# Kernel optimization log

Measured on AMD Instinct MI355X. Metric: run time of the kernel, lower is better.

Reference implementation:

```python
import jax, jax.numpy as jnp
import numpy as np

W_DIM = 512   # latent dim
CH = 512      # number of Fourier channels / output channels
SIZE = 64     # spatial size (square: size[0]=size[1])
SR = 64.0     # sampling_rate
BW = 2.0      # bandwidth
BATCH = 32


def setup_inputs() -> dict:
    key = jax.random.key(0)
    k1, k2, k3, k4, k5 = jax.random.split(key, 5)
    w = jax.random.normal(k1, (BATCH, W_DIM), jnp.float32)
    # affine FC params (weight_init=0 in original; use small random so t varies)
    affine_w = jax.random.normal(k2, (4, W_DIM), jnp.float32) * 0.1
    affine_b = jnp.array([1.0, 0.0, 0.0, 0.0], jnp.float32)
    # channel-mixing weight
    weight = jax.random.normal(k3, (CH, CH), jnp.float32)
    # freqs buffer init: randn, normalized by r*exp(r^2/4), scaled by bandwidth
    f = jax.random.normal(k4, (CH, 2), jnp.float32)
    radii = jnp.sqrt(jnp.sum(f * f, axis=1, keepdims=True))
    f = f / (radii * jnp.exp(radii * radii / 4.0)) * BW
    phases = jax.random.uniform(k5, (CH,), jnp.float32) - 0.5
    return {"w": w, "affine_w": affine_w, "affine_b": affine_b,
            "weight": weight, "freqs": f, "phases": phases}


def reference(w, affine_w, affine_b, weight, freqs, phases):
    # affine FC: FullyConnectedLayer with lr_multiplier=1 -> weight_gain = 1/sqrt(in)
    gain = np.float32(1.0 / np.sqrt(W_DIM))
    t = w @ (affine_w.T * gain) + affine_b                      # [N, 4]
    t = t / jnp.linalg.norm(t[:, :2], axis=1, keepdims=True)
    c, s, tx, ty = t[:, 0], t[:, 1], t[:, 2], t[:, 3]
    # combined transform = m_r @ m_t @ I; top-left 2x2 rotation block:
    R = jnp.stack([jnp.stack([c, -s], -1),
                   jnp.stack([s, c], -1)], axis=1)              # [N, 2, 2]
    # translation column of combined transform (m_r @ m_t)[:, :2, 2]
    trans = jnp.stack([-c * tx + s * ty, -s * tx - c * ty], -1) # [N, 2]
    ph = phases[None, :] + jnp.einsum('cd,nd->nc', freqs, trans)  # [N, C]
    fr = jnp.einsum('cd,nde->nce', freqs, R)                      # [N, C, 2]
    amp = jnp.clip(1.0 - (jnp.linalg.norm(fr, axis=2) - BW) / (SR / 2.0 - BW), 0.0, 1.0)  # [N, C]
    # affine_grid(theta, [1,1,H,W], align_corners=False): base coords (2i+1)/D - 1
    scale = np.float32(0.5 * SIZE / SR)
    xs = ((2.0 * jnp.arange(SIZE, dtype=jnp.float32) + 1.0) / SIZE - 1.0) * scale
    ys = ((2.0 * jnp.arange(SIZE, dtype=jnp.float32) + 1.0) / SIZE - 1.0) * scale
    grid = jnp.stack([jnp.broadcast_to(xs[None, :], (SIZE, SIZE)),
                      jnp.broadcast_to(ys[:, None], (SIZE, SIZE))], axis=-1)  # [H, W, 2]
    # per-pixel Fourier phase: [N, H, W, C]
    x = jnp.einsum('hwd,ncd->nhwc', grid, fr) + ph[:, None, None, :]
    x = jnp.sin(x * np.float32(2.0 * np.pi)) * amp[:, None, None, :]
    # channel projection, then to NCHW
    x = jnp.einsum('nhwc,kc->nkhw', x, weight * np.float32(1.0 / np.sqrt(CH)))
    return x  # [N, CH, H, W]
```

## Files before the change

### kernel.cpp

```cpp
#include <hip/hip_runtime.h>
#include <hip/hip_bf16.h>

#define WDIM 512
#define CHN  512
#define NB   32
#define SZ   64
#define MTOT 4096

typedef __attribute__((ext_vector_type(4))) float f32x4;
typedef __attribute__((ext_vector_type(8))) short short8;
typedef __attribute__((ext_vector_type(4))) int   int4v;
typedef __attribute__((ext_vector_type(4))) float float4v;

__global__ __launch_bounds__(512) void setup_kernel(
    const float* __restrict__ w,
    const float* __restrict__ affine_w,
    const float* __restrict__ affine_b,
    const float* __restrict__ freqs,
    const float* __restrict__ phases,
    float* __restrict__ frx_o, float* __restrict__ fry_o,
    float* __restrict__ pha_o, float* __restrict__ amp_o)
{
    const int n = blockIdx.x;
    const int tid = threadIdx.x;
    __shared__ float red[8][4];
    __shared__ float par[4];

    float wv = w[n * WDIM + tid];
    float p0 = wv * affine_w[0 * WDIM + tid];
    float p1 = wv * affine_w[1 * WDIM + tid];
    float p2 = wv * affine_w[2 * WDIM + tid];
    float p3 = wv * affine_w[3 * WDIM + tid];
    #pragma unroll
    for (int off = 32; off >= 1; off >>= 1) {
        p0 += __shfl_down(p0, off);
        p1 += __shfl_down(p1, off);
        p2 += __shfl_down(p2, off);
        p3 += __shfl_down(p3, off);
    }
    const int wave = tid >> 6;
    if ((tid & 63) == 0) {
        red[wave][0] = p0; red[wave][1] = p1;
        red[wave][2] = p2; red[wave][3] = p3;
    }
    __syncthreads();
    if (tid == 0) {
        const float gain = 0.04419417382415922f;
        float t[4];
        #pragma unroll
        for (int j = 0; j < 4; ++j) {
            float s = 0.0f;
            #pragma unroll
            for (int v = 0; v < 8; ++v) s += red[v][j];
            t[j] = s * gain + affine_b[j];
        }
        float inv = 1.0f / sqrtf(t[0] * t[0] + t[1] * t[1]);
        float c = t[0] * inv, s = t[1] * inv, tx = t[2] * inv, ty = t[3] * inv;
        par[0] = c;
        par[1] = s;
        par[2] = -c * tx + s * ty;
        par[3] = -s * tx - c * ty;
    }
    __syncthreads();
    const float c_ = par[0], s_ = par[1], tr0 = par[2], tr1 = par[3];
    const int ci = tid;
    float fx = freqs[ci * 2 + 0], fy = freqs[ci * 2 + 1];
    float frx = fx * c_ + fy * s_;
    float fry = -fx * s_ + fy * c_;
    float ph = phases[ci] + fx * tr0 + fy * tr1;
    float r = sqrtf(frx * frx + fry * fry);
    float amp = 1.0f - (r - 2.0f) * (1.0f / 30.0f);
    amp = fminf(fmaxf(amp, 0.0f), 1.0f);
    frx_o[n * CHN + ci] = frx;
    fry_o[n * CHN + ci] = fry;
    pha_o[n * CHN + ci] = ph;
    amp_o[n * CHN + ci] = amp;
}

__global__ __launch_bounds__(512) void table_kernel(
    const float* __restrict__ frx, const float* __restrict__ amp,
    float* __restrict__ SA, float* __restrict__ CA)
{
    const int n = blockIdx.x >> 6;
    const int w = blockIdx.x & 63;
    const int c = threadIdx.x;
    float f = frx[n * CHN + c];
    float a = amp[n * CHN + c];
    float xs = (float)(2 * w + 1) * (1.0f / 128.0f) - 0.5f;
    float arg = xs * f;
    size_t idx = ((size_t)(n * 64 + w)) * CHN + c;
    SA[idx] = a * __builtin_amdgcn_sinf(arg);
    CA[idx] = a * __builtin_amdgcn_cosf(arg);
}

__global__ __launch_bounds__(256) void wconv_kernel(
    const float* __restrict__ wsrc, __hip_bfloat16* __restrict__ wbf)
{
    int i = blockIdx.x * 256 + threadIdx.x;
    wbf[i] = __float2bfloat16(wsrc[i] * 0.04419417382415922f);
}

__global__ __launch_bounds__(256, 2) void fused_kernel(
    const float* __restrict__ fry, const float* __restrict__ pha,
    const float* __restrict__ SA, const float* __restrict__ CA,
    const __hip_bfloat16* __restrict__ wbf,
    float* __restrict__ out)
{
    __shared__ __align__(16) __hip_bfloat16 As[128 * 64];
    __shared__ __align__(16) __hip_bfloat16 Bs[128 * 64];
    __shared__ __align__(16) float sB[2][CHN];
    __shared__ __align__(16) float cB[2][CHN];

    const int tid = threadIdx.x;
    const int mb = blockIdx.x * 128;
    const int kb = blockIdx.y * 128;
    const int n  = blockIdx.z;
    const int h0 = mb >> 6;

    #pragma unroll
    for (int u = 0; u < 2; ++u) {
        int c = tid + u * 256;
        float fy = fry[n * CHN + c];
        float ph = pha[n * CHN + c];
        #pragma unroll
        for (int hh = 0; hh < 2; ++hh) {
            float ys = (float)(2 * (h0 + hh) + 1) * (1.0f / 128.0f) - 0.5f;
            float b = ys * fy + ph;
            sB[hh][c] = __builtin_amdgcn_sinf(b);
            cB[hh][c] = __builtin_amdgcn_cosf(b);
        }
    }

    const int lane = tid & 63;
    const int wid  = tid >> 6;
    const int ln15 = lane & 15;
    const int hi4  = lane >> 4;
    const int wk = (wid >> 1) * 64;
    const int wm = (wid & 1) * 64;

    const int cc0 = (tid & 7) * 8;
    const int rb  = tid >> 3;

    const float* saL = SA + ((size_t)(n * 64 + rb)) * CHN + cc0;
    const float* saH = SA + ((size_t)(n * 64 + rb + 32)) * CHN + cc0;
    const float* caL = CA + ((size_t)(n * 64 + rb)) * CHN + cc0;
    const float* caH = CA + ((size_t)(n * 64 + rb + 32)) * CHN + cc0;

    f32x4 acc[4][4];
    #pragma unroll
    for (int a = 0; a < 4; ++a)
        #pragma unroll
        for (int b = 0; b < 4; ++b)
            acc[a][b] = (f32x4)0.0f;

    #pragma unroll 1
    for (int kc = 0; kc < 8; ++kc) {
        const int c0 = kc * 64;
        __syncthreads();

        #pragma unroll
        for (int u = 0; u < 4; ++u) {
            int unit = u * 256 + tid;
            int row = unit >> 3;
            int cbyte = ((unit & 7) << 4) ^ ((row & 7) << 4);
            const __hip_bfloat16* src = wbf + (size_t)(kb + row) * CHN + c0 + (cbyte >> 1);
            char* ldsbase = (char*)Bs + (u * 256 + (wid << 6)) * 16;
            __builtin_amdgcn_global_load_lds(
                (const __attribute__((address_space(1))) unsigned int*)src,
                (__attribute__((address_space(3))) unsigned int*)ldsbase, 16, 0, 0);
        }

        float4v s0 = *(const float4v*)(saL + c0), s1 = *(const float4v*)(saL + c0 + 4);
        float4v s2 = *(const float4v*)(saH + c0), s3 = *(const float4v*)(saH + c0 + 4);
        float4v q0 = *(const float4v*)(caL + c0), q1 = *(const float4v*)(caL + c0 + 4);
        float4v q2 = *(const float4v*)(caH + c0), q3 = *(const float4v*)(caH + c0 + 4);
        #pragma unroll
        for (int i = 0; i < 4; ++i) {
            int m = rb + i * 32;
            int hh = i >> 1;
            float4v As0 = (i & 1) ? s2 : s0, As1 = (i & 1) ? s3 : s1;
            float4v Ac0 = (i & 1) ? q2 : q0, Ac1 = (i & 1) ? q3 : q1;
            float4v Bs0 = *(const float4v*)&sB[hh][c0 + cc0];
            float4v Bs1 = *(const float4v*)&sB[hh][c0 + cc0 + 4];
            float4v Bc0 = *(const float4v*)&cB[hh][c0 + cc0];
            float4v Bc1 = *(const float4v*)&cB[hh][c0 + cc0 + 4];
            union { __hip_bfloat16 h[8]; int4v v; } t;
            #pragma unroll
            for (int j = 0; j < 4; ++j)
                t.h[j] = __float2bfloat16(As0[j] * Bc0[j] + Ac0[j] * Bs0[j]);
            #pragma unroll
            for (int j = 0; j < 4; ++j)
                t.h[4 + j] = __float2bfloat16(As1[j] * Bc1[j] + Ac1[j] * Bs1[j]);
            *(int4v*)((char*)As + m * 128 + ((cc0 * 2) ^ ((m & 7) << 4))) = t.v;
        }
        __syncthreads();

        #pragma unroll
        for (int kk = 0; kk < 2; ++kk) {
            short8 wf[4], ff[4];
            #pragma unroll
            for (int ki = 0; ki < 4; ++ki) {
                int row = wk + ki * 16 + ln15;
                wf[ki] = *(const short8*)((char*)Bs + row * 128 +
                          (((kk * 32 + hi4 * 8) * 2) ^ ((row & 7) << 4)));
            }
            #pragma unroll
            for (int mj = 0; mj < 4; ++mj) {
                int m = wm + mj * 16 + ln15;
                ff[mj] = *(const short8*)((char*)As + m * 128 +
                          (((kk * 32 + hi4 * 8) * 2) ^ ((m & 7) << 4)));
            }
            #pragma unroll
            for (int ki = 0; ki < 4; ++ki)
                #pragma unroll
                for (int mj = 0; mj < 4; ++mj)
                    acc[ki][mj] = __builtin_amdgcn_mfma_f32_16x16x32_bf16(
                        wf[ki], ff[mj], acc[ki][mj], 0, 0, 0);
        }
    }

    #pragma unroll
    for (int ki = 0; ki < 4; ++ki) {
        #pragma unroll
        for (int mj = 0; mj < 4; ++mj) {
            int kg = kb + wk + ki * 16 + hi4 * 4;
            int mg = mb + wm + mj * 16 + ln15;
            float* op = out + ((size_t)n * CHN + kg) * MTOT + mg;
            #pragma unroll
            for (int r = 0; r < 4; ++r)
                op[(size_t)r * MTOT] = acc[ki][mj][r];
        }
    }
}

extern "C" void kernel_launch(void* const* d_in, const int* in_sizes, int n_in,
                              void* d_out, int out_size, void* d_ws, size_t ws_size,
                              hipStream_t stream) {
    const float* w        = (const float*)d_in[0];
    const float* affine_w = (const float*)d_in[1];
    const float* affine_b = (const float*)d_in[2];
    const float* weight   = (const float*)d_in[3];
    const float* freqs    = (const float*)d_in[4];
    const float* phases   = (const float*)d_in[5];
    float* out = (float*)d_out;

    char* ws = (char*)d_ws;
    float* frx = (float*)(ws + 0);
    float* fry = (float*)(ws + 65536);
    float* pha = (float*)(ws + 131072);
    float* amp = (float*)(ws + 196608);
    __hip_bfloat16* wbf = (__hip_bfloat16*)(ws + 262144);
    float* SA = (float*)(ws + 786432);
    float* CA = (float*)(ws + 786432 + 4194304);

    setup_kernel<<<NB, 512, 0, stream>>>(w, affine_w, affine_b, freqs, phases,
                                         frx, fry, pha, amp);
    table_kernel<<<NB * 64, 512, 0, stream>>>(frx, amp, SA, CA);
    wconv_kernel<<<(CHN * CHN) / 256, 256, 0, stream>>>(weight, wbf);

    dim3 grid(MTOT / 128, CHN / 128, NB);
    fused_kernel<<<grid, 256, 0, stream>>>(fry, pha, SA, CA, wbf, out);
}
```

Measured before the change: 120.8 us.

## Double-buffer LDS tiles in fused GEMM and merge table/weight-convert kernels

The fused kernel now keeps two LDS buffers for the feature and weight tiles. It prefetches the next K-chunk (async weight load plus SA/CA global loads) and builds its features while the current chunk's MFMAs run, which drops one barrier per iteration. The table and weight-conversion kernels are merged into one launch to save launch overhead. Doubling the LDS use (about 80KB per block) may limit occupancy under the 2-blocks-per-CU launch bound.

```diff
diff --git a/kernel.cpp b/kernel.cpp
--- a/kernel.cpp
+++ b/kernel.cpp
@@ -77,27 +77,28 @@
     amp_o[n * CHN + ci] = amp;
 }
 
-__global__ __launch_bounds__(512) void table_kernel(
+__global__ __launch_bounds__(512) void prep_kernel(
     const float* __restrict__ frx, const float* __restrict__ amp,
-    float* __restrict__ SA, float* __restrict__ CA)
+    const float* __restrict__ wsrc,
+    float* __restrict__ SA, float* __restrict__ CA,
+    __hip_bfloat16* __restrict__ wbf)
 {
-    const int n = blockIdx.x >> 6;
-    const int w = blockIdx.x & 63;
-    const int c = threadIdx.x;
-    float f = frx[n * CHN + c];
-    float a = amp[n * CHN + c];
-    float xs = (float)(2 * w + 1) * (1.0f / 128.0f) - 0.5f;
-    float arg = xs * f;
-    size_t idx = ((size_t)(n * 64 + w)) * CHN + c;
-    SA[idx] = a * __builtin_amdgcn_sinf(arg);
-    CA[idx] = a * __builtin_amdgcn_cosf(arg);
-}
-
-__global__ __launch_bounds__(256) void wconv_kernel(
-    const float* __restrict__ wsrc, __hip_bfloat16* __restrict__ wbf)
-{
-    int i = blockIdx.x * 256 + threadIdx.x;
-    wbf[i] = __float2bfloat16(wsrc[i] * 0.04419417382415922f);
+    const int b = blockIdx.x;
+    if (b < NB * 64) {
+        const int n = b >> 6;
+        const int w = b & 63;
+        const int c = threadIdx.x;
+        float f = frx[n * CHN + c];
+        float a = amp[n * CHN + c];
+        float xs = (float)(2 * w + 1) * (1.0f / 128.0f) - 0.5f;
+        float arg = xs * f;
+        size_t idx = ((size_t)(n * 64 + w)) * CHN + c;
+        SA[idx] = a * __builtin_amdgcn_sinf(arg);
+        CA[idx] = a * __builtin_amdgcn_cosf(arg);
+    } else {
+        int i = (b - NB * 64) * 512 + threadIdx.x;
+        wbf[i] = __float2bfloat16(wsrc[i] * 0.04419417382415922f);
+    }
 }
 
 __global__ __launch_bounds__(256, 2) void fused_kernel(
@@ -106,8 +107,8 @@
     const __hip_bfloat16* __restrict__ wbf,
     float* __restrict__ out)
 {
-    __shared__ __align__(16) __hip_bfloat16 As[128 * 64];
-    __shared__ __align__(16) __hip_bfloat16 Bs[128 * 64];
+    __shared__ __align__(16) __hip_bfloat16 As[2][128 * 64];
+    __shared__ __align__(16) __hip_bfloat16 Bs[2][128 * 64];
     __shared__ __align__(16) float sB[2][CHN];
     __shared__ __align__(16) float cB[2][CHN];
 
@@ -125,9 +126,9 @@
         #pragma unroll
         for (int hh = 0; hh < 2; ++hh) {
             float ys = (float)(2 * (h0 + hh) + 1) * (1.0f / 128.0f) - 0.5f;
-            float b = ys * fy + ph;
-            sB[hh][c] = __builtin_amdgcn_sinf(b);
-            cB[hh][c] = __builtin_amdgcn_cosf(b);
+            float bv = ys * fy + ph;
+            sB[hh][c] = __builtin_amdgcn_sinf(bv);
+            cB[hh][c] = __builtin_amdgcn_cosf(bv);
         }
     }
 
@@ -137,77 +138,79 @@
     const int hi4  = lane >> 4;
     const int wk = (wid >> 1) * 64;
     const int wm = (wid & 1) * 64;
-
     const int cc0 = (tid & 7) * 8;
     const int rb  = tid >> 3;
 
     const float* saL = SA + ((size_t)(n * 64 + rb)) * CHN + cc0;
-    const float* saH = SA + ((size_t)(n * 64 + rb + 32)) * CHN + cc0;
+    const float* saH = saL + 32 * CHN;
     const float* caL = CA + ((size_t)(n * 64 + rb)) * CHN + cc0;
-    const float* caH = CA + ((size_t)(n * 64 + rb + 32)) * CHN + cc0;
-
-    f32x4 acc[4][4];
-    #pragma unroll
-    for (int a = 0; a < 4; ++a)
-        #pragma unroll
-        for (int b = 0; b < 4; ++b)
-            acc[a][b] = (f32x4)0.0f;
-
-    #pragma unroll 1
-    for (int kc = 0; kc < 8; ++kc) {
-        const int c0 = kc * 64;
-        __syncthreads();
-
+    const float* caH = caL + 32 * CHN;
+
+    auto stageB = [&](int buf, int c0) {
         #pragma unroll
         for (int u = 0; u < 4; ++u) {
             int unit = u * 256 + tid;
             int row = unit >> 3;
             int cbyte = ((unit & 7) << 4) ^ ((row & 7) << 4);
             const __hip_bfloat16* src = wbf + (size_t)(kb + row) * CHN + c0 + (cbyte >> 1);
-            char* ldsbase = (char*)Bs + (u * 256 + (wid << 6)) * 16;
+            char* ldsbase = (char*)Bs[buf] + (u * 256 + (wid << 6)) * 16;
             __builtin_amdgcn_global_load_lds(
                 (const __attribute__((address_space(1))) unsigned int*)src,
                 (__attribute__((address_space(3))) unsigned int*)ldsbase, 16, 0, 0);
         }
-
-        float4v s0 = *(const float4v*)(saL + c0), s1 = *(const float4v*)(saL + c0 + 4);
-        float4v s2 = *(const float4v*)(saH + c0), s3 = *(const float4v*)(saH + c0 + 4);
-        float4v q0 = *(const float4v*)(caL + c0), q1 = *(const float4v*)(caL + c0 + 4);
-        float4v q2 = *(const float4v*)(caH + c0), q3 = *(const float4v*)(caH + c0 + 4);
+    };
+
+    float4v Ps0, Ps1, Ps2, Ps3, Pc0, Pc1, Pc2, Pc3;
+    auto loadP = [&](int c0) {
+        Ps0 = *(const float4v*)(saL + c0); Ps1 = *(const float4v*)(saL + c0 + 4);
+        Ps2 = *(const float4v*)(saH + c0); Ps3 = *(const float4v*)(saH + c0 + 4);
+        Pc0 = *(const float4v*)(caL + c0); Pc1 = *(const float4v*)(caL + c0 + 4);
+        Pc2 = *(const float4v*)(caH + c0); Pc3 = *(const float4v*)(caH + c0 + 4);
+    };
+
+    auto features = [&](int buf, int c0) {
         #pragma unroll
         for (int i = 0; i < 4; ++i) {
             int m = rb + i * 32;
             int hh = i >> 1;
-            float4v As0 = (i & 1) ? s2 : s0, As1 = (i & 1) ? s3 : s1;
-            float4v Ac0 = (i & 1) ? q2 : q0, Ac1 = (i & 1) ? q3 : q1;
-            float4v Bs0 = *(const float4v*)&sB[hh][c0 + cc0];
-            float4v Bs1 = *(const float4v*)&sB[hh][c0 + cc0 + 4];
-            float4v Bc0 = *(const float4v*)&cB[hh][c0 + cc0];
-            float4v Bc1 = *(const float4v*)&cB[hh][c0 + cc0 + 4];
+            float4v A0 = (i & 1) ? Ps2 : Ps0, A1 = (i & 1) ? Ps3 : Ps1;
+            float4v C0 = (i & 1) ? Pc2 : Pc0, C1 = (i & 1) ? Pc3 : Pc1;
+            float4v B0 = *(const float4v*)&sB[hh][c0 + cc0];
+            float4v B1 = *(const float4v*)&sB[hh][c0 + cc0 + 4];
+            float4v D0 = *(const float4v*)&cB[hh][c0 + cc0];
+            float4v D1 = *(const float4v*)&cB[hh][c0 + cc0 + 4];
             union { __hip_bfloat16 h[8]; int4v v; } t;
             #pragma unroll
             for (int j = 0; j < 4; ++j)
-                t.h[j] = __float2bfloat16(As0[j] * Bc0[j] + Ac0[j] * Bs0[j]);
+                t.h[j] = __float2bfloat16(A0[j] * D0[j] + C0[j] * B0[j]);
             #pragma unroll
             for (int j = 0; j < 4; ++j)
-                t.h[4 + j] = __float2bfloat16(As1[j] * Bc1[j] + Ac1[j] * Bs1[j]);
-            *(int4v*)((char*)As + m * 128 + ((cc0 * 2) ^ ((m & 7) << 4))) = t.v;
-        }
-        __syncthreads();
-
+                t.h[4 + j] = __float2bfloat16(A1[j] * D1[j] + C1[j] * B1[j]);
+            *(int4v*)((char*)As[buf] + m * 128 + ((cc0 * 2) ^ ((m & 7) << 4))) = t.v;
+        }
+    };
+
+    f32x4 acc[4][4];
+    #pragma unroll
+    for (int a = 0; a < 4; ++a)
+        #pragma unroll
+        for (int b = 0; b < 4; ++b)
+            acc[a][b] = (f32x4)0.0f;
+
+    auto mfmaStep = [&](int buf) {
         #pragma unroll
         for (int kk = 0; kk < 2; ++kk) {
             short8 wf[4], ff[4];
             #pragma unroll
             for (int ki = 0; ki < 4; ++ki) {
                 int row = wk + ki * 16 + ln15;
-                wf[ki] = *(const short8*)((char*)Bs + row * 128 +
+                wf[ki] = *(const short8*)((char*)Bs[buf] + row * 128 +
                           (((kk * 32 + hi4 * 8) * 2) ^ ((row & 7) << 4)));
             }
             #pragma unroll
             for (int mj = 0; mj < 4; ++mj) {
                 int m = wm + mj * 16 + ln15;
-                ff[mj] = *(const short8*)((char*)As + m * 128 +
+                ff[mj] = *(const short8*)((char*)As[buf] + m * 128 +
                           (((kk * 32 + hi4 * 8) * 2) ^ ((m & 7) << 4)));
             }
             #pragma unroll
@@ -216,6 +219,26 @@
                 for (int mj = 0; mj < 4; ++mj)
                     acc[ki][mj] = __builtin_amdgcn_mfma_f32_16x16x32_bf16(
                         wf[ki], ff[mj], acc[ki][mj], 0, 0, 0);
+        }
+    };
+
+    stageB(0, 0);
+    loadP(0);
+    __syncthreads();
+    features(0, 0);
+    __syncthreads();
+
+    #pragma unroll 1
+    for (int kc = 0; kc < 8; ++kc) {
+        const int cur = kc & 1;
+        if (kc < 7) {
+            stageB(cur ^ 1, (kc + 1) * 64);
+            loadP((kc + 1) * 64);
+        }
+        mfmaStep(cur);
+        if (kc < 7) {
+            features(cur ^ 1, (kc + 1) * 64);
+            __syncthreads();
         }
     }
 
@@ -255,8 +278,8 @@
 
     setup_kernel<<<NB, 512, 0, stream>>>(w, affine_w, affine_b, freqs, phases,
                                          frx, fry, pha, amp);
-    table_kernel<<<NB * 64, 512, 0, stream>>>(frx, amp, SA, CA);
-    wconv_kernel<<<(CHN * CHN) / 256, 256, 0, stream>>>(weight, wbf);
+    prep_kernel<<<NB * 64 + (CHN * CHN) / 512, 512, 0, stream>>>(
+        frx, amp, weight, SA, CA, wbf);
 
     dim3 grid(MTOT / 128, CHN / 128, NB);
     fused_kernel<<<grid, 256, 0, stream>>>(fry, pha, SA, CA, wbf, out);
```

Result: slower. 133.0 us (+10.0%).
